# Optimization experiments

Measured on AMD Instinct MI355X. Metric: run time of the kernel, lower is better.

The kernel has to match this reference:

```python
import jax, jax.numpy as jnp
import numpy as np

D_MODEL, N_HEADS, D_HEAD = 1024, 16, 64
IGNORE = -1e5

def setup_inputs() -> dict:
    key = jax.random.key(0)
    ks = jax.random.split(key, 5)
    std = 0.02
    return {
        "resid_pre": jax.random.normal(ks[0], (4, 2048, D_MODEL), dtype=jnp.float32),
        "W_Q": jax.random.normal(ks[1], (N_HEADS, D_MODEL, D_HEAD), dtype=jnp.float32) * std,
        "W_K": jax.random.normal(ks[2], (N_HEADS, D_MODEL, D_HEAD), dtype=jnp.float32) * std,
        "W_V": jax.random.normal(ks[3], (N_HEADS, D_MODEL, D_HEAD), dtype=jnp.float32) * std,
        "W_O": jax.random.normal(ks[4], (N_HEADS, D_HEAD, D_MODEL), dtype=jnp.float32) * std,
        "b_Q": jnp.zeros((N_HEADS, D_HEAD), dtype=jnp.float32),
        "b_K": jnp.zeros((N_HEADS, D_HEAD), dtype=jnp.float32),
        "b_V": jnp.zeros((N_HEADS, D_HEAD), dtype=jnp.float32),
        "b_O": jnp.zeros((D_MODEL,), dtype=jnp.float32),
    }

def reference(resid_pre, W_Q, W_K, W_V, W_O, b_Q, b_K, b_V, b_O):
    # q/k/v: [batch, posn, n_heads, d_head]
    q = jnp.einsum("hmd,bsm->bshd", W_Q, resid_pre) + b_Q
    k = jnp.einsum("hmd,bsm->bshd", W_K, resid_pre) + b_K
    v = jnp.einsum("hmd,bsm->bshd", W_V, resid_pre) + b_V
    # scores: [batch, n_heads, posn_q, posn_k]
    scores = jnp.einsum("bqhd,bkhd->bhqk", q, k) / jnp.sqrt(jnp.float32(D_HEAD))
    S = resid_pre.shape[1]
    causal = jnp.tril(jnp.ones((S, S), dtype=bool))  # keep where True
    scores = jnp.where(causal, scores, jnp.float32(IGNORE))
    probs = jax.nn.softmax(scores, axis=-1)
    z = jnp.einsum("bhqk,bkhd->bqhd", probs, v)  # [batch, posn_q, n_heads, d_head]
    # project each head to d_model and sum over heads, then add b_O
    attn_out = jnp.einsum("hdm,bqhd->bqm", W_O, z) + b_O
    return attn_out
```

## Files before the change

kernel.cpp:

```cpp
#include <hip/hip_runtime.h>

typedef __bf16 bf16;
typedef __attribute__((ext_vector_type(8))) __bf16 bf16x8;
typedef __attribute__((ext_vector_type(4))) float f32x4;

__device__ __forceinline__ void gload_lds16(const void* g, void* l) {
  __builtin_amdgcn_global_load_lds(
      (const __attribute__((address_space(1))) unsigned int*)(g),
      (__attribute__((address_space(3))) unsigned int*)(l),
      16, 0, 0);
}

__device__ __forceinline__ float exp2_hw(float x) {
  float r; asm("v_exp_f32 %0, %1" : "=v"(r) : "v"(x)); return r;
}
__device__ __forceinline__ unsigned cvtpk_bf16(float a, float b) {
  unsigned r; asm("v_cvt_pk_bf16_f32 %0, %1, %2" : "=v"(r) : "v"(a), "v"(b)); return r;
}

#define QSCALE 0.1803368867f


__global__ __launch_bounds__(256) void pack_x(const float* __restrict__ x, bf16* __restrict__ o) {
  int i = (blockIdx.x * 256 + threadIdx.x) * 8;
  float4 a = *(const float4*)(x + i);
  float4 b = *(const float4*)(x + i + 4);
  bf16x8 v;
  v[0] = (bf16)a.x; v[1] = (bf16)a.y; v[2] = (bf16)a.z; v[3] = (bf16)a.w;
  v[4] = (bf16)b.x; v[5] = (bf16)b.y; v[6] = (bf16)b.z; v[7] = (bf16)b.w;
  *(bf16x8*)(o + i) = v;
}

__global__ __launch_bounds__(256) void pack_w(const float* __restrict__ WQ, const float* __restrict__ WK,
                                              const float* __restrict__ WV, bf16* __restrict__ Wt) {
  int bid = blockIdx.x;
  int p = bid >> 8, h = (bid >> 4) & 15, k0 = (bid & 15) * 64;
  const float* src = (p == 0 ? WQ : p == 1 ? WK : WV) + h * 65536;
  float scl = (p == 0) ? QSCALE : 1.0f;
  __shared__ float tile[64][65];
  int t = threadIdx.x, c = t & 63, r4 = t >> 6;
#pragma unroll
  for (int rr = 0; rr < 16; ++rr) {
    int k = r4 + rr * 4;
    tile[k][c] = src[(k0 + k) * 64 + c];
  }
  __syncthreads();
#pragma unroll
  for (int rr = 0; rr < 16; ++rr) {
    int d = r4 + rr * 4;
    Wt[(p * 1024 + h * 64 + d) * 1024 + k0 + c] = (bf16)(tile[c][d] * scl);
  }
}

__global__ __launch_bounds__(256) void pack_wo(const float* __restrict__ WO, bf16* __restrict__ Wt) {
  int bid = blockIdx.x;
  int r0 = (bid >> 4) * 64, c0 = (bid & 15) * 64;
  __shared__ float tile[64][65];
  int t = threadIdx.x, c = t & 63, r4 = t >> 6;
#pragma unroll
  for (int rr = 0; rr < 16; ++rr) {
    int r = r4 + rr * 4;
    tile[r][c] = WO[(r0 + r) * 1024 + c0 + c];
  }
  __syncthreads();
#pragma unroll
  for (int rr = 0; rr < 16; ++rr) {
    int m = r4 + rr * 4;
    Wt[(c0 + m) * 1024 + r0 + c] = (bf16)tile[c][m];
  }
}

__global__ __launch_bounds__(256) void pack_bias(const float* __restrict__ bQ, const float* __restrict__ bK,
                                                 const float* __restrict__ bV, float* __restrict__ o) {
  int i = blockIdx.x * 256 + threadIdx.x;
  if (i < 3072) {
    int p = i >> 10, j = i & 1023;
    float v = (p == 0 ? bQ : p == 1 ? bK : bV)[j];
    o[i] = (p == 0) ? v * QSCALE : v;
  }
}

template <int OUTF32>
__global__ __launch_bounds__(256, 2) void gemm_bt(const bf16* __restrict__ A, const bf16* __restrict__ Bt,
                                                  const float* __restrict__ bias, void* __restrict__ Cv,
                                                  int M, int N, int K) {
  __shared__ bf16 As[128 * 64];
  __shared__ bf16 Bs[128 * 64];
  int tid = threadIdx.x;
  int wv = tid >> 6, ln = tid & 63, lr = ln & 15, lh = ln >> 4;
  int wr = wv >> 1, wc = wv & 1;
  int row0 = blockIdx.y * 128, col0 = blockIdx.x * 128;
  int ss = (ln & 7) ^ (ln >> 3);
  const char* ga = (const char*)(A + (long)(row0 + wv * 32 + (ln >> 3)) * K) + ss * 16;
  const char* gb = (const char*)(Bt + (long)(col0 + wv * 32 + (ln >> 3)) * K) + ss * 16;
  long rowskip = (long)8 * K * 2;
  f32x4 acc[4][4] = {};
  for (int k0 = 0; k0 < K; k0 += 64) {
#pragma unroll
    for (int i = 0; i < 4; ++i) {
      gload_lds16(ga + (long)k0 * 2 + i * rowskip, (char*)As + (wv * 32 + i * 8) * 128);
      gload_lds16(gb + (long)k0 * 2 + i * rowskip, (char*)Bs + (wv * 32 + i * 8) * 128);
    }
    __syncthreads();
    bf16x8 af[4][2], bfr[4][2];
#pragma unroll
    for (int mi = 0; mi < 4; ++mi)
#pragma unroll
      for (int ks = 0; ks < 2; ++ks) {
        int row = wr * 64 + mi * 16 + lr;
        int o = row * 128 + (((ks * 4 + lh) ^ (row & 7)) << 4);
        af[mi][ks] = *(const bf16x8*)((const char*)As + o);
      }
#pragma unroll
    for (int ni = 0; ni < 4; ++ni)
#pragma unroll
      for (int ks = 0; ks < 2; ++ks) {
        int row = wc * 64 + ni * 16 + lr;
        int o = row * 128 + (((ks * 4 + lh) ^ (row & 7)) << 4);
        bfr[ni][ks] = *(const bf16x8*)((const char*)Bs + o);
      }
    __builtin_amdgcn_s_setprio(1);
#pragma unroll
    for (int ks = 0; ks < 2; ++ks)
#pragma unroll
      for (int mi = 0; mi < 4; ++mi)
#pragma unroll
        for (int ni = 0; ni < 4; ++ni)
          acc[mi][ni] = __builtin_amdgcn_mfma_f32_16x16x32_bf16(af[mi][ks], bfr[ni][ks], acc[mi][ni], 0, 0, 0);
    __builtin_amdgcn_s_setprio(0);
    __syncthreads();
  }
#pragma unroll
  for (int mi = 0; mi < 4; ++mi) {
    int row = row0 + wr * 64 + mi * 16 + lh * 4;
#pragma unroll
    for (int ni = 0; ni < 4; ++ni) {
      int col = col0 + wc * 64 + ni * 16 + lr;
      float bvv = bias[col];
#pragma unroll
      for (int r = 0; r < 4; ++r) {
        float v = acc[mi][ni][r] + bvv;
        if (OUTF32) ((float*)Cv)[(long)(row + r) * N + col] = v;
        else        ((bf16*)Cv)[(long)(row + r) * N + col] = (bf16)v;
      }
    }
  }
}

__global__ __launch_bounds__(256, 2) void flash(const bf16* __restrict__ Qkv, bf16* __restrict__ Z) {
  __shared__ bf16 Vt[2][64 * 64];
  __shared__ unsigned char Pl[4][4096];
  const float MASKV = -144269.5041f;
  int bid = blockIdx.x;
  int pair = bid >> 6;
  int bh = (bid & 7) * 8 + ((bid >> 3) & 7);
  int b = bh >> 4, h = bh & 15;
  int tid = threadIdx.x;
  int wv = tid >> 6, ln = tid & 63, lr = ln & 15, lh = ln >> 4;
  const bf16* Qg = Qkv + (long)b * 2048 * 3072 + h * 64;
  const bf16* Kg = Qg + 1024;
  const bf16* Vg = Qg + 2048;
  int vs0 = (tid >> 3) * 2, vd0 = (tid & 7) * 8;
  char* pw = (char*)Pl[wv];

  bf16x8 v0, v1;
  auto loadV = [&](int kvrow0) {
    v0 = *(const bf16x8*)(Vg + (long)(kvrow0 + vs0) * 3072 + vd0);
    v1 = *(const bf16x8*)(Vg + (long)(kvrow0 + vs0 + 1) * 3072 + vd0);
  };
  auto writeV = [&](bf16* vd) {
#pragma unroll
    for (int j = 0; j < 8; ++j) {
      int d = vd0 + j;
      int o = (d * 128 + vs0 * 2) ^ ((((d & 7) ^ (d >> 3)) & 7) << 4);
      unsigned int pk = (unsigned int)__builtin_bit_cast(unsigned short, (bf16)v0[j])
                      | ((unsigned int)__builtin_bit_cast(unsigned short, (bf16)v1[j]) << 16);
      *(unsigned int*)((char*)vd + o) = pk;
    }
  };

#pragma unroll 1
  for (int half = 0; half < 2; ++half) {
    int qt = half ? 15 - pair : pair;
    int q0 = qt * 128;
    int nt = 2 * (qt + 1);
    loadV(0);
    bf16x8 bq[2][2];
#pragma unroll
    for (int mi = 0; mi < 2; ++mi)
#pragma unroll
      for (int ks = 0; ks < 2; ++ks)
        bq[mi][ks] = *(const bf16x8*)(Qg + (long)(q0 + wv * 32 + mi * 16 + lr) * 3072 + ks * 32 + lh * 8);
    writeV(Vt[0]);
    __syncthreads();

    f32x4 oa[4][2] = {};
    float m_st[2], l_st[2];
    m_st[0] = m_st[1] = -1e30f;
    l_st[0] = l_st[1] = 0.f;

    int cur = 0;
    for (int t = 0; t < nt; ++t) {
      int kv0 = t * 64;
      bool more = (t + 1 < nt);
      bf16x8 kf[4][2];
#pragma unroll
      for (int n = 0; n < 4; ++n)
#pragma unroll
        for (int ks = 0; ks < 2; ++ks)
          kf[n][ks] = *(const bf16x8*)(Kg + (long)(kv0 + n * 16 + lr) * 3072 + ks * 32 + lh * 8);
      if (more) loadV(kv0 + 64);
      f32x4 sc[2][4];
      __builtin_amdgcn_s_setprio(1);
#pragma unroll
      for (int mi = 0; mi < 2; ++mi)
#pragma unroll
        for (int n = 0; n < 4; ++n) {
          f32x4 zacc = {0.f, 0.f, 0.f, 0.f};
          zacc = __builtin_amdgcn_mfma_f32_16x16x32_bf16(kf[n][0], bq[mi][0], zacc, 0, 0, 0);
          zacc = __builtin_amdgcn_mfma_f32_16x16x32_bf16(kf[n][1], bq[mi][1], zacc, 0, 0, 0);
          sc[mi][n] = zacc;
        }
      __builtin_amdgcn_s_setprio(0);
      if (kv0 + 63 > q0) {
#pragma unroll
        for (int mi = 0; mi < 2; ++mi) {
          int qrow = q0 + wv * 32 + mi * 16 + lr;
#pragma unroll
          for (int n = 0; n < 4; ++n) {
            int kvb = kv0 + n * 16 + lh * 4;
#pragma unroll
            for (int r = 0; r < 4; ++r)
              if (kvb + r > qrow) sc[mi][n][r] = MASKV;
          }
        }
      }
#pragma unroll
      for (int mi = 0; mi < 2; ++mi) {
        float mx = sc[mi][0][0];
#pragma unroll
        for (int n = 0; n < 4; ++n)
#pragma unroll
          for (int r = 0; r < 4; ++r) mx = fmaxf(mx, sc[mi][n][r]);
        mx = fmaxf(mx, __shfl_xor(mx, 16));
        mx = fmaxf(mx, __shfl_xor(mx, 32));
        if (!__all(mx <= m_st[mi] + 8.0f)) {
          float mn = fmaxf(m_st[mi], mx);
          float resc = exp2_hw(m_st[mi] - mn);
          m_st[mi] = mn;
          l_st[mi] *= resc;
#pragma unroll
          for (int n2 = 0; n2 < 4; ++n2)
#pragma unroll
            for (int r = 0; r < 4; ++r) oa[n2][mi][r] *= resc;
        }
        float s = 0.f;
#pragma unroll
        for (int n = 0; n < 4; ++n)
#pragma unroll
          for (int r = 0; r < 4; ++r) {
            float p = exp2_hw(sc[mi][n][r] - m_st[mi]);
            sc[mi][n][r] = p;
            s += p;
          }
        s += __shfl_xor(s, 16);
        s += __shfl_xor(s, 32);
        l_st[mi] += s;
      }
#pragma unroll
      for (int mi = 0; mi < 2; ++mi) {
        int row = mi * 16 + lr;
#pragma unroll
        for (int n = 0; n < 4; ++n) {
          int addr = row * 128 + ((n * 32 + lh * 8) ^ ((row & 7) << 4));
          uint2 val = { cvtpk_bf16(sc[mi][n][0], sc[mi][n][1]),
                        cvtpk_bf16(sc[mi][n][2], sc[mi][n][3]) };
          *(uint2*)(pw + addr) = val;
        }
      }
      if (more) writeV(Vt[cur ^ 1]);
      bf16x8 pa[2][2];
#pragma unroll
      for (int mi = 0; mi < 2; ++mi)
#pragma unroll
        for (int ks = 0; ks < 2; ++ks) {
          int row = mi * 16 + lr;
          int o = row * 128 + (((ks * 4 + lh) ^ (row & 7)) << 4);
          pa[mi][ks] = *(const bf16x8*)(pw + o);
        }
      __builtin_amdgcn_s_setprio(1);
#pragma unroll
      for (int n2 = 0; n2 < 4; ++n2) {
        int row = n2 * 16 + lr;
        int o0 = row * 128 + ((((0 + lh) ^ (row & 7) ^ ((row >> 3) & 7)) & 7) << 4);
        int o1 = row * 128 + ((((4 + lh) ^ (row & 7) ^ ((row >> 3) & 7)) & 7) << 4);
        bf16x8 vf0 = *(const bf16x8*)((const char*)Vt[cur] + o0);
        bf16x8 vf1 = *(const bf16x8*)((const char*)Vt[cur] + o1);
#pragma unroll
        for (int mi = 0; mi < 2; ++mi) {
          oa[n2][mi] = __builtin_amdgcn_mfma_f32_16x16x32_bf16(vf0, pa[mi][0], oa[n2][mi], 0, 0, 0);
          oa[n2][mi] = __builtin_amdgcn_mfma_f32_16x16x32_bf16(vf1, pa[mi][1], oa[n2][mi], 0, 0, 0);
        }
      }
      __builtin_amdgcn_s_setprio(0);
      __syncthreads();
      cur ^= 1;
    }
#pragma unroll
    for (int mi = 0; mi < 2; ++mi) {
      float inv = 1.0f / l_st[mi];
      int q = q0 + wv * 32 + mi * 16 + lr;
      bf16* zb = Z + ((long)b * 2048 + q) * 1024 + h * 64 + lh * 4;
#pragma unroll
      for (int n2 = 0; n2 < 4; ++n2) {
        uint2 o2 = { cvtpk_bf16(oa[n2][mi][0] * inv, oa[n2][mi][1] * inv),
                     cvtpk_bf16(oa[n2][mi][2] * inv, oa[n2][mi][3] * inv) };
        *(uint2*)(zb + n2 * 16) = o2;
      }
    }
  }
}

extern "C" void kernel_launch(void* const* d_in, const int* in_sizes, int n_in,
                              void* d_out, int out_size, void* d_ws, size_t ws_size,
                              hipStream_t stream) {
  const float* resid = (const float*)d_in[0];
  const float* WQ = (const float*)d_in[1];
  const float* WK = (const float*)d_in[2];
  const float* WV = (const float*)d_in[3];
  const float* WO = (const float*)d_in[4];
  const float* bQ = (const float*)d_in[5];
  const float* bK = (const float*)d_in[6];
  const float* bV = (const float*)d_in[7];
  const float* bO = (const float*)d_in[8];
  char* ws = (char*)d_ws;
  bf16*  Xb      = (bf16*)ws;
  bf16*  Z       = (bf16*)ws;
  bf16*  Wqkv    = (bf16*)(ws + 16777216);
  bf16*  Wot     = (bf16*)(ws + 16777216);
  float* biasqkv = (float*)(ws + 23068672);
  bf16*  QKVo    = (bf16*)(ws + 23085056);

  pack_x<<<4096, 256, 0, stream>>>(resid, Xb);
  pack_w<<<768, 256, 0, stream>>>(WQ, WK, WV, Wqkv);
  pack_bias<<<12, 256, 0, stream>>>(bQ, bK, bV, biasqkv);
  gemm_bt<0><<<dim3(24, 64), 256, 0, stream>>>(Xb, Wqkv, biasqkv, QKVo, 8192, 3072, 1024);
  pack_wo<<<256, 256, 0, stream>>>(WO, Wot);
  flash<<<512, 256, 0, stream>>>(QKVo, Z);
  gemm_bt<1><<<dim3(8, 64), 256, 0, stream>>>(Z, Wot, bO, d_out, 8192, 1024, 1024);
}
```

Before: 264.8 us.

## Fuse input pack kernels and use 256x128 GEMM tiles with 8 waves

```diff
diff --git a/kernel.cpp b/kernel.cpp
--- a/kernel.cpp
+++ b/kernel.cpp
@@ -20,35 +20,48 @@
 
 #define QSCALE 0.1803368867f
 
-
-__global__ __launch_bounds__(256) void pack_x(const float* __restrict__ x, bf16* __restrict__ o) {
-  int i = (blockIdx.x * 256 + threadIdx.x) * 8;
-  float4 a = *(const float4*)(x + i);
-  float4 b = *(const float4*)(x + i + 4);
-  bf16x8 v;
-  v[0] = (bf16)a.x; v[1] = (bf16)a.y; v[2] = (bf16)a.z; v[3] = (bf16)a.w;
-  v[4] = (bf16)b.x; v[5] = (bf16)b.y; v[6] = (bf16)b.z; v[7] = (bf16)b.w;
-  *(bf16x8*)(o + i) = v;
-}
-
-__global__ __launch_bounds__(256) void pack_w(const float* __restrict__ WQ, const float* __restrict__ WK,
-                                              const float* __restrict__ WV, bf16* __restrict__ Wt) {
+__global__ __launch_bounds__(256) void pack_all(const float* __restrict__ x,
+                                                const float* __restrict__ WQ, const float* __restrict__ WK,
+                                                const float* __restrict__ WV,
+                                                const float* __restrict__ bQ, const float* __restrict__ bK,
+                                                const float* __restrict__ bV,
+                                                bf16* __restrict__ Xb, bf16* __restrict__ Wt,
+                                                float* __restrict__ biaso) {
+  __shared__ float tile[64][65];
   int bid = blockIdx.x;
-  int p = bid >> 8, h = (bid >> 4) & 15, k0 = (bid & 15) * 64;
-  const float* src = (p == 0 ? WQ : p == 1 ? WK : WV) + h * 65536;
-  float scl = (p == 0) ? QSCALE : 1.0f;
-  __shared__ float tile[64][65];
-  int t = threadIdx.x, c = t & 63, r4 = t >> 6;
-#pragma unroll
-  for (int rr = 0; rr < 16; ++rr) {
-    int k = r4 + rr * 4;
-    tile[k][c] = src[(k0 + k) * 64 + c];
-  }
-  __syncthreads();
-#pragma unroll
-  for (int rr = 0; rr < 16; ++rr) {
-    int d = r4 + rr * 4;
-    Wt[(p * 1024 + h * 64 + d) * 1024 + k0 + c] = (bf16)(tile[c][d] * scl);
+  int t = threadIdx.x;
+  if (bid < 4096) {
+    int i = (bid * 256 + t) * 8;
+    float4 a = *(const float4*)(x + i);
+    float4 b = *(const float4*)(x + i + 4);
+    bf16x8 v;
+    v[0] = (bf16)a.x; v[1] = (bf16)a.y; v[2] = (bf16)a.z; v[3] = (bf16)a.w;
+    v[4] = (bf16)b.x; v[5] = (bf16)b.y; v[6] = (bf16)b.z; v[7] = (bf16)b.w;
+    *(bf16x8*)(Xb + i) = v;
+  } else if (bid < 4864) {
+    int wb = bid - 4096;
+    int p = wb >> 8, h = (wb >> 4) & 15, k0 = (wb & 15) * 64;
+    const float* src = (p == 0 ? WQ : p == 1 ? WK : WV) + h * 65536;
+    float scl = (p == 0) ? QSCALE : 1.0f;
+    int c = t & 63, r4 = t >> 6;
+#pragma unroll
+    for (int rr = 0; rr < 16; ++rr) {
+      int k = r4 + rr * 4;
+      tile[k][c] = src[(k0 + k) * 64 + c];
+    }
+    __syncthreads();
+#pragma unroll
+    for (int rr = 0; rr < 16; ++rr) {
+      int d = r4 + rr * 4;
+      Wt[(p * 1024 + h * 64 + d) * 1024 + k0 + c] = (bf16)(tile[c][d] * scl);
+    }
+  } else {
+    int i = (bid - 4864) * 256 + t;
+    if (i < 3072) {
+      int p = i >> 10, j = i & 1023;
+      float v = (p == 0 ? bQ : p == 1 ? bK : bV)[j];
+      biaso[i] = (p == 0) ? v * QSCALE : v;
+    }
   }
 }
 
@@ -70,37 +83,28 @@
   }
 }
 
-__global__ __launch_bounds__(256) void pack_bias(const float* __restrict__ bQ, const float* __restrict__ bK,
-                                                 const float* __restrict__ bV, float* __restrict__ o) {
-  int i = blockIdx.x * 256 + threadIdx.x;
-  if (i < 3072) {
-    int p = i >> 10, j = i & 1023;
-    float v = (p == 0 ? bQ : p == 1 ? bK : bV)[j];
-    o[i] = (p == 0) ? v * QSCALE : v;
-  }
-}
-
 template <int OUTF32>
-__global__ __launch_bounds__(256, 2) void gemm_bt(const bf16* __restrict__ A, const bf16* __restrict__ Bt,
+__global__ __launch_bounds__(512, 2) void gemm_bt(const bf16* __restrict__ A, const bf16* __restrict__ Bt,
                                                   const float* __restrict__ bias, void* __restrict__ Cv,
                                                   int M, int N, int K) {
-  __shared__ bf16 As[128 * 64];
+  __shared__ bf16 As[256 * 64];
   __shared__ bf16 Bs[128 * 64];
   int tid = threadIdx.x;
   int wv = tid >> 6, ln = tid & 63, lr = ln & 15, lh = ln >> 4;
   int wr = wv >> 1, wc = wv & 1;
-  int row0 = blockIdx.y * 128, col0 = blockIdx.x * 128;
+  int row0 = blockIdx.y * 256, col0 = blockIdx.x * 128;
   int ss = (ln & 7) ^ (ln >> 3);
   const char* ga = (const char*)(A + (long)(row0 + wv * 32 + (ln >> 3)) * K) + ss * 16;
-  const char* gb = (const char*)(Bt + (long)(col0 + wv * 32 + (ln >> 3)) * K) + ss * 16;
+  const char* gb = (const char*)(Bt + (long)(col0 + wv * 16 + (ln >> 3)) * K) + ss * 16;
   long rowskip = (long)8 * K * 2;
   f32x4 acc[4][4] = {};
   for (int k0 = 0; k0 < K; k0 += 64) {
 #pragma unroll
-    for (int i = 0; i < 4; ++i) {
+    for (int i = 0; i < 4; ++i)
       gload_lds16(ga + (long)k0 * 2 + i * rowskip, (char*)As + (wv * 32 + i * 8) * 128);
-      gload_lds16(gb + (long)k0 * 2 + i * rowskip, (char*)Bs + (wv * 32 + i * 8) * 128);
-    }
+#pragma unroll
+    for (int i = 0; i < 2; ++i)
+      gload_lds16(gb + (long)k0 * 2 + i * rowskip, (char*)Bs + (wv * 16 + i * 8) * 128);
     __syncthreads();
     bf16x8 af[4][2], bfr[4][2];
 #pragma unroll
@@ -341,11 +345,9 @@
   float* biasqkv = (float*)(ws + 23068672);
   bf16*  QKVo    = (bf16*)(ws + 23085056);
 
-  pack_x<<<4096, 256, 0, stream>>>(resid, Xb);
-  pack_w<<<768, 256, 0, stream>>>(WQ, WK, WV, Wqkv);
-  pack_bias<<<12, 256, 0, stream>>>(bQ, bK, bV, biasqkv);
-  gemm_bt<0><<<dim3(24, 64), 256, 0, stream>>>(Xb, Wqkv, biasqkv, QKVo, 8192, 3072, 1024);
+  pack_all<<<4876, 256, 0, stream>>>(resid, WQ, WK, WV, bQ, bK, bV, Xb, Wqkv, biasqkv);
+  gemm_bt<0><<<dim3(24, 32), 512, 0, stream>>>(Xb, Wqkv, biasqkv, QKVo, 8192, 3072, 1024);
   pack_wo<<<256, 256, 0, stream>>>(WO, Wot);
   flash<<<512, 256, 0, stream>>>(QKVo, Z);
-  gemm_bt<1><<<dim3(8, 64), 256, 0, stream>>>(Z, Wot, bO, d_out, 8192, 1024, 1024);
-}
+  gemm_bt<1><<<dim3(8, 32), 512, 0, stream>>>(Z, Wot, bO, d_out, 8192, 1024, 1024);
+}
```

Result: slower. 298.0 us (+12.5%).
